# Optimization experiments

Hardware: AMD Instinct MI355X
Metric: run time of the kernel (lower is better)

The kernel has to match this reference:

```python
import jax, jax.numpy as jnp
import numpy as np

MIN_CURV = 1e-06
MIN_NORM = 1e-15

def _norm(x):
    return jnp.clip(jnp.linalg.norm(x, axis=-1, keepdims=True), MIN_NORM, None)

def lorentz_expmap0(v, c):
    sqrt_c = jnp.sqrt(c)
    vn = _norm(v)
    x0 = jnp.cosh(sqrt_c * vn) / sqrt_c
    xs = jnp.sinh(sqrt_c * vn) * v / (sqrt_c * vn)
    return jnp.concatenate([x0, xs], axis=-1)

def lorentz_logmap0(x, c):
    sqrt_c = jnp.sqrt(c)
    x0 = x[..., 0:1]
    xs = x[..., 1:]
    xs_norm = _norm(xs)
    theta = jnp.arccosh(jnp.clip(sqrt_c * x0, 1.0 + 1e-07, None))
    return theta / (sqrt_c * xs_norm) * xs

def lorentz_project(x, c):
    spatial = x[..., 1:]
    sq = jnp.sum(spatial * spatial, axis=-1, keepdims=True)
    x0 = jnp.clip(jnp.sqrt(sq + 1.0 / c), MIN_NORM, None)
    return jnp.concatenate([x0, spatial], axis=-1)

def givens_rotation(x, angles):
    x0 = x[..., 0:1]
    xs = x[..., 1:]
    cos_a = jnp.cos(angles)
    sin_a = jnp.sin(angles)
    xe = xs[..., 0::2]
    xo = xs[..., 1::2]
    ne = cos_a * xe - sin_a * xo
    no = sin_a * xe + cos_a * xo
    xr = jnp.stack([ne, no], axis=-1).reshape(xs.shape)
    return jnp.concatenate([x0, xr], axis=-1)

def setup_inputs() -> dict:
    key = jax.random.key(0)
    ks = jax.random.split(key, 16)
    N_NODE, E, B = 50000, 500000, 64
    IN_DIM, OUT_DIM, ATTN_DIM, N_REL = 128, 128, 128, 200
    N_EMB = 2 * N_REL + 1  # 401
    hidden = jax.random.normal(ks[0], (N_NODE, IN_DIM), dtype=jnp.float32)
    q_sub = jax.random.randint(ks[1], (B,), 0, N_NODE)
    q_rel = jax.random.randint(ks[2], (B,), 0, N_EMB)
    r_idx = jax.random.randint(ks[3], (E,), 0, B)
    rel = jax.random.randint(ks[4], (E,), 0, N_EMB)
    sub = jax.random.randint(ks[5], (E,), 0, N_NODE)
    obj = jax.random.randint(ks[6], (E,), 0, N_NODE)
    zeros = jnp.zeros((E,), dtype=jnp.int32)
    edges = jnp.stack([r_idx, zeros, rel, zeros, sub, obj], axis=1)
    rela_embed = jax.random.normal(ks[7], (N_EMB, IN_DIM), dtype=jnp.float32)
    rel_angles = jax.random.uniform(ks[8], (N_EMB, IN_DIM // 2), minval=-0.1, maxval=0.1, dtype=jnp.float32)
    curvature = jnp.array(1.0, dtype=jnp.float32)
    Ws_w = jax.random.normal(ks[9], (ATTN_DIM, IN_DIM), dtype=jnp.float32) * 0.05
    Wr_w = jax.random.normal(ks[10], (ATTN_DIM, IN_DIM), dtype=jnp.float32) * 0.05
    Wqr_w = jax.random.normal(ks[11], (ATTN_DIM, IN_DIM), dtype=jnp.float32) * 0.05
    Wqr_b = jax.random.normal(ks[12], (ATTN_DIM,), dtype=jnp.float32) * 0.05
    Wattn_w = jax.random.normal(ks[13], (1, ATTN_DIM), dtype=jnp.float32) * 0.05
    Wh_w = jax.random.normal(ks[14], (OUT_DIM, IN_DIM), dtype=jnp.float32) * 0.05
    return {"hidden": hidden, "rela_embed": rela_embed, "rel_angles": rel_angles,
            "curvature": curvature, "Ws_w": Ws_w, "Wr_w": Wr_w, "Wqr_w": Wqr_w,
            "Wqr_b": Wqr_b, "Wattn_w": Wattn_w, "Wh_w": Wh_w,
            "q_sub": q_sub, "q_rel": q_rel, "edges": edges,
            "n_node": N_NODE, "old_nodes_new_idx": jnp.arange(N_NODE)}

def reference(hidden, rela_embed, rel_angles, curvature, Ws_w, Wr_w, Wqr_w, Wqr_b,
              Wattn_w, Wh_w, q_sub, q_rel, edges, n_node, old_nodes_new_idx):
    sub = edges[:, 4]
    rel = edges[:, 2]
    obj = edges[:, 5]
    r_idx = edges[:, 0]
    hs = hidden[sub]                      # [E, in_dim]
    hr = rela_embed[rel]                  # [E, in_dim]
    h_qr = rela_embed[q_rel][r_idx]       # [E, in_dim]
    pre = jax.nn.relu(hs @ Ws_w.T + hr @ Wr_w.T + h_qr @ Wqr_w.T + Wqr_b)
    alpha = jax.nn.sigmoid(pre @ Wattn_w.T)  # [E, 1]
    c = jnp.clip(curvature, MIN_CURV, None)
    mess_tangent = hs + hr
    mess_L = lorentz_expmap0(mess_tangent, c)          # [E, in_dim+1]
    mess_L = givens_rotation(mess_L, rel_angles[rel])
    mess2 = lorentz_logmap0(mess_L, c)                 # [E, in_dim]
    message = mess2 * alpha
    message_agg = jax.ops.segment_sum(message, obj, num_segments=n_node)
    a = message_agg @ Wh_w.T                           # [n_node, out_dim]
    a_L = lorentz_expmap0(a, c)
    # act is identity; project back to hyperboloid and log-map
    a_L = lorentz_project(jnp.concatenate([a_L[..., 0:1], a_L[..., 1:]], axis=-1), c)
    hidden_new = lorentz_logmap0(a_L, c)
    return hidden_new
```

## Files before the change

### kernel.cpp

```cpp
#include <hip/hip_runtime.h>
#include <math.h>

#define D 128
#define CAP 36
#define NQ 64

typedef _Float16 f16x8 __attribute__((ext_vector_type(8)));
typedef _Float16 f16x4 __attribute__((ext_vector_type(4)));
typedef _Float16 f16x2 __attribute__((ext_vector_type(2)));
typedef float    f32x4 __attribute__((ext_vector_type(4)));

union H8 { f16x8 v; f16x4 q[2]; f16x2 p[4]; _Float16 f[8]; };
union H4 { f16x4 v; f16x2 p[2]; _Float16 f[4]; };
union U2 { f16x2 v; unsigned u; };

__device__ __forceinline__ float fdot2f(f16x2 a, f16x2 b, float c){
  return __builtin_amdgcn_fdot2(a, b, c, false);
}
__device__ __forceinline__ f16x2 relu2(f16x2 x){
  f16x2 r;
  r[0] = x[0] > (_Float16)0 ? x[0] : (_Float16)0;
  r[1] = x[1] > (_Float16)0 ? x[1] : (_Float16)0;
  return r;
}
__device__ __forceinline__ f16x2 negHi(f16x2 x){
  U2 u; u.v = x; u.u ^= 0x80000000u; return u.v;
}
__device__ __forceinline__ f16x2 swapH(f16x2 x){
  U2 u; u.v = x; u.u = (u.u >> 16) | (u.u << 16); return u.v;
}


__device__ __forceinline__ void hgemm_core16(const _Float16* __restrict__ A,
                                             const _Float16* __restrict__ W,
                                             int arow, f32x4 acc[8], int quad, int lo){
  #pragma unroll
  for (int kt=0;kt<4;kt++){
    f16x8 a = *(const f16x8*)(A + (size_t)arow*D + kt*32 + quad*8);
    #pragma unroll
    for (int nt=0;nt<8;nt++){
      f16x8 b = *(const f16x8*)(W + (size_t)(nt*16 + lo)*D + kt*32 + quad*8);
      acc[nt] = __builtin_amdgcn_mfma_f32_16x16x32_f16(a, b, acc[nt], 0, 0, 0);
    }
  }
}

__device__ __forceinline__ void store_wpart(_Float16* __restrict__ O, f32x4 acc[8],
                                            int m0, int quad, int lo, int M){
  int r0 = m0 + quad*4;
  #pragma unroll
  for (int i=0;i<4;i++){
    int r = r0 + i;
    if (r < M){
      H4 s1, s2;
      #pragma unroll
      for (int nt=0;nt<4;nt++){
        s1.f[nt] = (_Float16)acc[nt][i];
        s2.f[nt] = (_Float16)acc[nt+4][i];
      }
      *(f16x4*)(O + (size_t)r*256 + lo*16 + 4)  = s1.v;
      *(f16x4*)(O + (size_t)r*256 + lo*16 + 12) = s2.v;
    }
  }
}

__global__ __launch_bounds__(256) void k_prep(
    const float* __restrict__ rela, const float* __restrict__ rel_angles,
    const float* __restrict__ Ws, const float* __restrict__ Wr,
    const float* __restrict__ Wh, const float* __restrict__ Wqr,
    _Float16* __restrict__ rela16, _Float16* __restrict__ relhq,
    _Float16* __restrict__ relcs, _Float16* __restrict__ Ws16,
    _Float16* __restrict__ Wr16, _Float16* __restrict__ Wh16,
    _Float16* __restrict__ Wqr16, int* __restrict__ cnt,
    int NEMB, int NN){
  int idx = blockIdx.x*256 + threadIdx.x;
  int T1 = NEMB*32;
  if (idx < T1){
    int r = idx >> 5, l = idx & 31;
    float4 hv = *(const float4*)(rela + (size_t)r*D + l*4);
    f16x4 h = { (_Float16)hv.x, (_Float16)hv.y, (_Float16)hv.z, (_Float16)hv.w };
    *(f16x4*)(rela16 + (size_t)r*D + l*4) = h;
    *(f16x4*)(relhq  + (size_t)r*256 + l*8) = h;
    float2 an = *(const float2*)(rel_angles + (size_t)r*(D/2) + l*2);
    float c0 = cosf(an.x), s0 = sinf(an.x);
    float c1 = cosf(an.y), s1 = sinf(an.y);
    H4 cs;
    cs.f[0]=(_Float16)c0; cs.f[1]=(_Float16)s0;
    cs.f[2]=(_Float16)c1; cs.f[3]=(_Float16)s1;
    *(f16x4*)(relcs + (size_t)r*128 + l*4) = cs.v;
    return;
  }
  int j = idx - T1;
  if (j < 4*D*D/4){
    const float* src = (j < 4096) ? Ws : (j < 8192) ? Wr : (j < 12288) ? Wh : Wqr;
    _Float16*    dst = (j < 4096) ? Ws16 : (j < 8192) ? Wr16 : (j < 12288) ? Wh16 : Wqr16;
    int o = (j & 4095)*4;
    float4 v = *(const float4*)(src + o);
    f16x4 h = { (_Float16)v.x, (_Float16)v.y, (_Float16)v.z, (_Float16)v.w };
    *(f16x4*)(dst + o) = h;
    return;
  }
  j -= 4*D*D/4;
  if (j < NN + NQ*64) cnt[j] = 0;
}

__global__ __launch_bounds__(256) void k_mega(
    const int* __restrict__ edges, int* __restrict__ cnt, int* __restrict__ bucket,
    int E, const float* __restrict__ hidden, const _Float16* __restrict__ Ws16,
    _Float16* __restrict__ hw16, int NN,
    const _Float16* __restrict__ rela16, const _Float16* __restrict__ Wr16,
    _Float16* __restrict__ relhq, int NEMB, int SB, int GH, int G1,
    const _Float16* __restrict__ Wqr16, const float* __restrict__ Wqr_b,
    const int* __restrict__ q_rel, _Float16* __restrict__ hqw16){
  int b = blockIdx.x;
  if (b < SB){
    int e0 = (b*256 + threadIdx.x)*4;
    if (e0 >= E) return;
    if (e0 + 3 < E){
      const int4* q = (const int4*)(edges + (size_t)e0*6);
      int4 q0=q[0], q1=q[1], q2=q[2], q3=q[3], q4=q[4], q5=q[5];
      int key0 = q1.x | (q0.z << 17) | (q0.x << 26);
      int key1 = q2.z | (q2.x << 17) | (q1.z << 26);
      int key2 = q4.x | (q3.z << 17) | (q3.x << 26);
      int key3 = q5.z | (q5.x << 17) | (q4.z << 26);
      int p0 = atomicAdd(cnt + q1.y, 1);
      int p1 = atomicAdd(cnt + q2.w, 1);
      int p2 = atomicAdd(cnt + q4.y, 1);
      int p3 = atomicAdd(cnt + q5.w, 1);
      if (p0 < CAP) bucket[q1.y*CAP + p0] = key0;
      if (p1 < CAP) bucket[q2.w*CAP + p1] = key1;
      if (p2 < CAP) bucket[q4.y*CAP + p2] = key2;
      if (p3 < CAP) bucket[q5.w*CAP + p3] = key3;
    } else {
      for (int u=0; u<4; u++){
        int e = e0 + u;
        if (e < E){
          const int* er = edges + (size_t)e*6;
          int key = er[4] | (er[2] << 17) | (er[0] << 26);
          int pos = atomicAdd(cnt + er[5], 1);
          if (pos < CAP) bucket[er[5]*CAP + pos] = key;
        }
      }
    }
  } else if (b < SB + GH){
    int bb = b - SB;
    int wave = threadIdx.x >> 6;
    int lane = threadIdx.x & 63;
    int quad = lane >> 4, lo = lane & 15;
    int m0 = bb*64 + wave*16;
    int arow = min(m0 + lo, NN-1);
    f32x4 acc[8];
    #pragma unroll
    for (int nt=0;nt<8;nt++) acc[nt] = (f32x4){0.f,0.f,0.f,0.f};
    H8 hpack[4];
    #pragma unroll
    for (int kt=0;kt<4;kt++){
      float4 a0 = *(const float4*)(hidden + (size_t)arow*D + kt*32 + quad*8);
      float4 a1 = *(const float4*)(hidden + (size_t)arow*D + kt*32 + quad*8 + 4);
      H8 a;
      a.f[0]=(_Float16)a0.x; a.f[1]=(_Float16)a0.y; a.f[2]=(_Float16)a0.z; a.f[3]=(_Float16)a0.w;
      a.f[4]=(_Float16)a1.x; a.f[5]=(_Float16)a1.y; a.f[6]=(_Float16)a1.z; a.f[7]=(_Float16)a1.w;
      hpack[kt] = a;
      #pragma unroll
      for (int nt=0;nt<8;nt++){
        f16x8 bb2 = *(const f16x8*)(Ws16 + (size_t)(nt*16 + lo)*D + kt*32 + quad*8);
        acc[nt] = __builtin_amdgcn_mfma_f32_16x16x32_f16(a.v, bb2, acc[nt], 0, 0, 0);
      }
    }
    if (m0 + lo < NN){
      #pragma unroll
      for (int kt=0;kt<4;kt++){
        int g = kt*8 + quad*2;
        *(f16x4*)(hw16 + (size_t)arow*256 + g*8)     = hpack[kt].q[0];
        *(f16x4*)(hw16 + (size_t)arow*256 + (g+1)*8) = hpack[kt].q[1];
      }
    }
    store_wpart(hw16, acc, m0, quad, lo, NN);
  } else if (b < SB + GH + G1){
    int bb = b - SB - GH;
    int wave = threadIdx.x >> 6;
    int lane = threadIdx.x & 63;
    int quad = lane >> 4, lo = lane & 15;
    int m0 = bb*64 + wave*16;
    int arow = min(m0 + lo, NEMB-1);
    f32x4 acc[8];
    #pragma unroll
    for (int nt=0;nt<8;nt++) acc[nt] = (f32x4){0.f,0.f,0.f,0.f};
    hgemm_core16(rela16, Wr16, arow, acc, quad, lo);
    store_wpart(relhq, acc, m0, quad, lo, NEMB);
  } else {
    int wave = threadIdx.x >> 6;
    int lane = threadIdx.x & 63;
    int quad = lane >> 4, lo = lane & 15;
    int m0 = wave*16;
    int arow = q_rel[m0 + lo];
    f32x4 acc[8];
    #pragma unroll
    for (int nt=0;nt<8;nt++) acc[nt] = (f32x4){0.f,0.f,0.f,0.f};
    hgemm_core16(rela16, Wqr16, arow, acc, quad, lo);
    int r0 = m0 + quad*4;
    #pragma unroll
    for (int nt=0;nt<8;nt++){
      int c = nt*16 + lo;
      float bia = Wqr_b[c];
      int p = ((c & 15) << 3) + (c >> 4);
      #pragma unroll
      for (int i=0;i<4;i++){
        int r = r0 + i;
        hqw16[r*128 + p] = (_Float16)(acc[nt][i] + bia);
      }
    }
  }
}

struct P {
  H8 h0,h1,h2,h3;
  int4 q;
  float m1,m2,m3;
};

__device__ __forceinline__ void pload(const int* __restrict__ bk, int g, int deg,
    const _Float16* __restrict__ hw16, unsigned lh8, P& o){
  int4 q = *(const int4*)(bk + (g << 2));
  int base = g << 2;
  bool v1 = base + 1 < deg, v2 = base + 2 < deg, v3 = base + 3 < deg;
  if (!v1) q.y = 0;
  if (!v2) q.z = 0;
  if (!v3) q.w = 0;
  o.q = q;
  o.m1 = v1 ? 1.f : 0.f;
  o.m2 = v2 ? 1.f : 0.f;
  o.m3 = v3 ? 1.f : 0.f;
  o.h0.v = *(const f16x8*)(hw16 + ((((unsigned)q.x) & 0x1FFFF) << 8) + lh8);
  o.h1.v = *(const f16x8*)(hw16 + ((((unsigned)q.y) & 0x1FFFF) << 8) + lh8);
  o.h2.v = *(const f16x8*)(hw16 + ((((unsigned)q.z) & 0x1FFFF) << 8) + lh8);
  o.h3.v = *(const f16x8*)(hw16 + ((((unsigned)q.w) & 0x1FFFF) << 8) + lh8);
}

__device__ __forceinline__ void gcompute(const P& A,
    const _Float16* __restrict__ relcs, const _Float16* __restrict__ relhq,
    const _Float16* shq,
    unsigned lh8, unsigned lh4, int l, f16x2 wa01, f16x2 wa23,
    float& ax, float& ay, float& az, float& aw){
  unsigned r0 = ((unsigned)A.q.x >> 17) & 0x1FF, i0 = (unsigned)A.q.x >> 26;
  unsigned r1 = ((unsigned)A.q.y >> 17) & 0x1FF, i1 = (unsigned)A.q.y >> 26;
  unsigned r2 = ((unsigned)A.q.z >> 17) & 0x1FF, i2 = (unsigned)A.q.z >> 26;
  unsigned r3 = ((unsigned)A.q.w >> 17) & 0x1FF, i3 = (unsigned)A.q.w >> 26;
  H4 c0,c1,c2,c3; H8 e0,e1,e2,e3; H4 w0,w1,w2,w3;
  c0.v = *(const f16x4*)(relcs + (r0 << 7) + lh4);
  c1.v = *(const f16x4*)(relcs + (r1 << 7) + lh4);
  c2.v = *(const f16x4*)(relcs + (r2 << 7) + lh4);
  c3.v = *(const f16x4*)(relcs + (r3 << 7) + lh4);
  e0.v = *(const f16x8*)(relhq + (r0 << 8) + lh8);
  e1.v = *(const f16x8*)(relhq + (r1 << 8) + lh8);
  e2.v = *(const f16x8*)(relhq + (r2 << 8) + lh8);
  e3.v = *(const f16x8*)(relhq + (r3 << 8) + lh8);
  w0.v = *(const f16x4*)(shq + (i0 << 7) + lh4);
  w1.v = *(const f16x4*)(shq + (i1 << 7) + lh4);
  w2.v = *(const f16x4*)(shq + (i2 << 7) + lh4);
  w3.v = *(const f16x4*)(shq + (i3 << 7) + lh4);
  f16x2 ta, tb;
  ta = relu2(A.h0.p[2] + e0.p[2] + w0.p[0]); tb = relu2(A.h0.p[3] + e0.p[3] + w0.p[1]);
  float s0 = fdot2f(ta, wa01, fdot2f(tb, wa23, 0.f));
  ta = relu2(A.h1.p[2] + e1.p[2] + w1.p[0]); tb = relu2(A.h1.p[3] + e1.p[3] + w1.p[1]);
  float s1 = fdot2f(ta, wa01, fdot2f(tb, wa23, 0.f));
  ta = relu2(A.h2.p[2] + e2.p[2] + w2.p[0]); tb = relu2(A.h2.p[3] + e2.p[3] + w2.p[1]);
  float s2 = fdot2f(ta, wa01, fdot2f(tb, wa23, 0.f));
  ta = relu2(A.h3.p[2] + e3.p[2] + w3.p[0]); tb = relu2(A.h3.p[3] + e3.p[3] + w3.p[1]);
  float s3 = fdot2f(ta, wa01, fdot2f(tb, wa23, 0.f));
  bool b0 = (l & 1) != 0, b1 = (l & 2) != 0;
  float x01 = b0 ? s1 : s0, y01 = b0 ? s0 : s1;
  float r01 = x01 + __shfl_xor(y01, 1);
  float x23 = b0 ? s3 : s2, y23 = b0 ? s2 : s3;
  float r23 = x23 + __shfl_xor(y23, 1);
  float xa = b1 ? r23 : r01, ya = b1 ? r01 : r23;
  float rr = xa + __shfl_xor(ya, 2);
  rr += __shfl_xor(rr, 4);
  rr += __shfl_xor(rr, 8);
  rr += __shfl_xor(rr, 16);
  float av = __builtin_amdgcn_rcpf(1.f + __expf(-rr));
  float aB = __shfl_xor(av, 1);
  float aC = __shfl_xor(av, 2);
  float aD = __shfl_xor(aB, 2);
  float g0 = b0 ? aB : av, g1 = b0 ? av : aB, g2 = b0 ? aD : aC, g3 = b0 ? aC : aD;
  float al0 = b1 ? g2 : g0, al1 = b1 ? g3 : g1, al2 = b1 ? g0 : g2, al3 = b1 ? g1 : g3;
  al1 *= A.m1; al2 *= A.m2; al3 *= A.m3;
  f16x2 v01, v23;
  v01 = A.h0.p[0] + e0.p[0]; v23 = A.h0.p[1] + e0.p[1];
  float dx0 = fdot2f(negHi(c0.p[0]), v01, 0.f), dy0 = fdot2f(swapH(c0.p[0]), v01, 0.f);
  float dz0 = fdot2f(negHi(c0.p[1]), v23, 0.f), dw0 = fdot2f(swapH(c0.p[1]), v23, 0.f);
  v01 = A.h1.p[0] + e1.p[0]; v23 = A.h1.p[1] + e1.p[1];
  float dx1 = fdot2f(negHi(c1.p[0]), v01, 0.f), dy1 = fdot2f(swapH(c1.p[0]), v01, 0.f);
  float dz1 = fdot2f(negHi(c1.p[1]), v23, 0.f), dw1 = fdot2f(swapH(c1.p[1]), v23, 0.f);
  v01 = A.h2.p[0] + e2.p[0]; v23 = A.h2.p[1] + e2.p[1];
  float dx2 = fdot2f(negHi(c2.p[0]), v01, 0.f), dy2 = fdot2f(swapH(c2.p[0]), v01, 0.f);
  float dz2 = fdot2f(negHi(c2.p[1]), v23, 0.f), dw2 = fdot2f(swapH(c2.p[1]), v23, 0.f);
  v01 = A.h3.p[0] + e3.p[0]; v23 = A.h3.p[1] + e3.p[1];
  float dx3 = fdot2f(negHi(c3.p[0]), v01, 0.f), dy3 = fdot2f(swapH(c3.p[0]), v01, 0.f);
  float dz3 = fdot2f(negHi(c3.p[1]), v23, 0.f), dw3 = fdot2f(swapH(c3.p[1]), v23, 0.f);
  ax += al0*dx0 + al1*dx1 + al2*dx2 + al3*dx3;
  ay += al0*dy0 + al1*dy1 + al2*dy2 + al3*dy3;
  az += al0*dz0 + al1*dz1 + al2*dz2 + al3*dz3;
  aw += al0*dw0 + al1*dw1 + al2*dw2 + al3*dw3;
}

__global__ __launch_bounds__(256, 4) void k_aggregate(
    const _Float16* __restrict__ hw16, const _Float16* __restrict__ relcs,
    const _Float16* __restrict__ relhq, const _Float16* __restrict__ hqw16,
    const float* __restrict__ Wattn, const int* __restrict__ cnt,
    const int* __restrict__ bucket, _Float16* __restrict__ agg16, int NN,
    int* __restrict__ wq, int B){
  __shared__ _Float16 shq[64*128];
  int t = threadIdx.x;
  int nb = min(B, 64) * 128;
  for (int i = t*8; i < nb; i += 256*8)
    *(f16x8*)(shq + i) = *(const f16x8*)(hqw16 + i);
  __syncthreads();

  int l = t & 31;
  unsigned lh8 = (unsigned)l*8, lh4 = (unsigned)l*4;
  unsigned p0 = (unsigned)l*4;
  float w0 = Wattn[(((p0+0)&7)<<4) + ((p0+0)>>3)];
  float w1 = Wattn[(((p0+1)&7)<<4) + ((p0+1)>>3)];
  float w2 = Wattn[(((p0+2)&7)<<4) + ((p0+2)>>3)];
  float w3 = Wattn[(((p0+3)&7)<<4) + ((p0+3)>>3)];
  f16x2 wa01 = { (_Float16)w0, (_Float16)w1 };
  f16x2 wa23 = { (_Float16)w2, (_Float16)w3 };

  int cid  = blockIdx.x & (NQ-1);
  int qpc  = NN / NQ, rem = NN % NQ;
  int base = cid * qpc + min(cid, rem);
  int len  = qpc + (cid < rem ? 1 : 0);
  int* myq = wq + cid * 64;

  for (;;){
    int i;
    if (l == 0) i = atomicAdd(myq, 1);
    i = __shfl(i, 0, 32);
    if (i >= len) break;
    int n = base + i;

    int deg = min(cnt[n], CAP);
    const int* bk = bucket + n*CAP;
    float ax=0.f, ay=0.f, az=0.f, aw=0.f;

    int ng = (deg + 3) >> 2;
    if (ng){
      P A, Bf;
      pload(bk, 0, deg, hw16, lh8, A);
      int g = 0;
      for (;;){
        if (g + 1 < ng) pload(bk, g+1, deg, hw16, lh8, Bf);
        gcompute(A, relcs, relhq, shq, lh8, lh4, l, wa01, wa23, ax, ay, az, aw);
        if (++g >= ng) break;
        if (g + 1 < ng) pload(bk, g+1, deg, hw16, lh8, A);
        gcompute(Bf, relcs, relhq, shq, lh8, lh4, l, wa01, wa23, ax, ay, az, aw);
        if (++g >= ng) break;
      }
    }

    f16x4 o = { (_Float16)ax, (_Float16)ay, (_Float16)az, (_Float16)aw };
    *(f16x4*)(agg16 + ((size_t)n << 7) + lh4) = o;
  }
}

__global__ __launch_bounds__(256) void k_hgemm0(const _Float16* __restrict__ A,
                                                const _Float16* __restrict__ W,
                                                float* __restrict__ O, int M){
  int wave = threadIdx.x >> 6;
  int lane = threadIdx.x & 63;
  int quad = lane >> 4, lo = lane & 15;
  int m0 = blockIdx.x*64 + wave*16;
  int arow = min(m0 + lo, M-1);
  f32x4 acc[8];
  #pragma unroll
  for (int nt=0;nt<8;nt++) acc[nt] = (f32x4){0.f,0.f,0.f,0.f};
  hgemm_core16(A, W, arow, acc, quad, lo);
  int r0 = m0 + quad*4;
  #pragma unroll
  for (int nt=0;nt<8;nt++){
    int c = nt*16 + lo;
    #pragma unroll
    for (int i=0;i<4;i++){
      int r = r0 + i;
      if (r < M) O[(size_t)r*D + c] = acc[nt][i];
    }
  }
}

extern "C" void kernel_launch(void* const* d_in, const int* in_sizes, int n_in,
                              void* d_out, int out_size, void* d_ws, size_t ws_size,
                              hipStream_t stream){
  const float* hidden     = (const float*)d_in[0];
  const float* rela       = (const float*)d_in[1];
  const float* rel_angles = (const float*)d_in[2];
  const float* Ws         = (const float*)d_in[4];
  const float* Wr         = (const float*)d_in[5];
  const float* Wqr        = (const float*)d_in[6];
  const float* Wqr_b      = (const float*)d_in[7];
  const float* Wattn      = (const float*)d_in[8];
  const float* Wh         = (const float*)d_in[9];
  const int*   q_rel      = (const int*)d_in[11];
  const int*   edges      = (const int*)d_in[12];

  int NN   = in_sizes[0] / D;
  int NEMB = in_sizes[1] / D;
  int B    = in_sizes[11];
  int E    = in_sizes[12] / 6;

  char* p = (char*)d_ws;
  auto alloc = [&](size_t bytes)->char*{
    char* r = p; p += (bytes + 255) & ~(size_t)255; return r;
  };
  _Float16* hw16   = (_Float16*)alloc((size_t)NN*256*2);
  _Float16* agg16  = (_Float16*)alloc((size_t)NN*D*2);
  _Float16* rela16 = (_Float16*)alloc((size_t)NEMB*D*2);
  _Float16* relhq  = (_Float16*)alloc((size_t)NEMB*256*2);
  _Float16* relcs  = (_Float16*)alloc((size_t)NEMB*128*2);
  _Float16* hqw16  = (_Float16*)alloc((size_t)B*D*2);
  _Float16* Ws16   = (_Float16*)alloc((size_t)D*D*2);
  _Float16* Wr16   = (_Float16*)alloc((size_t)D*D*2);
  _Float16* Wh16   = (_Float16*)alloc((size_t)D*D*2);
  _Float16* Wqr16  = (_Float16*)alloc((size_t)D*D*2);
  int*      cnt    = (int*)alloc((size_t)(NN + NQ*64)*4);
  int*      bucket = (int*)alloc((size_t)NN*CAP*4);

  int smallN = NEMB*32 + 4*D*D/4 + NN + NQ*64;
  int PA = (smallN + 255)/256;
  k_prep<<<PA, 256, 0, stream>>>(rela, rel_angles, Ws, Wr, Wh, Wqr,
                                 rela16, relhq, relcs, Ws16, Wr16, Wh16,
                                 Wqr16, cnt, NEMB, NN);

  int SB = (E + 1023)/1024;
  int GH = (NN + 63)/64;
  int G1 = (NEMB + 63)/64;
  k_mega<<<SB + GH + G1 + 1, 256, 0, stream>>>(edges, cnt, bucket, E, hidden,
                                               Ws16, hw16, NN, rela16, Wr16,
                                               relhq, NEMB, SB, GH, G1,
                                               Wqr16, Wqr_b, q_rel, hqw16);

  k_aggregate<<<2048, 256, 0, stream>>>(hw16, relcs, relhq, hqw16,
                                        Wattn, cnt, bucket, agg16, NN,
                                        cnt + NN, B);
  k_hgemm0<<<(NN+63)/64, 256, 0, stream>>>(agg16, Wh16, (float*)d_out, NN);
}
```

Baseline: 225.3 us.

## Split edge scatter out of merged GEMM kernel into separate launch

Moves the edge bucketing scatter out of the combined mega kernel into its own kernel, launched just before a kernel that holds only the three GEMM branches. The scatter now handles one edge per thread with scalar loads, where it used to handle four edges per thread with int4 vector loads. This separates the atomic-heavy scatter from the MFMA GEMM blocks, possibly to avoid interference or register-pressure coupling between them. In exchange it adds a kernel launch and serializes work that used to run concurrently in one grid.

```diff
diff --git a/kernel.cpp b/kernel.cpp
--- a/kernel.cpp
+++ b/kernel.cpp
@@ -104,50 +104,31 @@
   if (j < NN + NQ*64) cnt[j] = 0;
 }
 
-__global__ __launch_bounds__(256) void k_mega(
-    const int* __restrict__ edges, int* __restrict__ cnt, int* __restrict__ bucket,
-    int E, const float* __restrict__ hidden, const _Float16* __restrict__ Ws16,
+__global__ __launch_bounds__(256) void k_scatter(
+    const int* __restrict__ edges, int* __restrict__ cnt,
+    int* __restrict__ bucket, int E){
+  int e = blockIdx.x*256 + threadIdx.x;
+  if (e >= E) return;
+  const int* er = edges + (size_t)e*6;
+  int key = er[4] | (er[2] << 17) | (er[0] << 26);
+  int obj = er[5];
+  int pos = atomicAdd(cnt + obj, 1);
+  if (pos < CAP) bucket[obj*CAP + pos] = key;
+}
+
+__global__ __launch_bounds__(256) void k_gemms(
+    const float* __restrict__ hidden, const _Float16* __restrict__ Ws16,
     _Float16* __restrict__ hw16, int NN,
     const _Float16* __restrict__ rela16, const _Float16* __restrict__ Wr16,
-    _Float16* __restrict__ relhq, int NEMB, int SB, int GH, int G1,
+    _Float16* __restrict__ relhq, int NEMB, int GH, int G1,
     const _Float16* __restrict__ Wqr16, const float* __restrict__ Wqr_b,
     const int* __restrict__ q_rel, _Float16* __restrict__ hqw16){
   int b = blockIdx.x;
-  if (b < SB){
-    int e0 = (b*256 + threadIdx.x)*4;
-    if (e0 >= E) return;
-    if (e0 + 3 < E){
-      const int4* q = (const int4*)(edges + (size_t)e0*6);
-      int4 q0=q[0], q1=q[1], q2=q[2], q3=q[3], q4=q[4], q5=q[5];
-      int key0 = q1.x | (q0.z << 17) | (q0.x << 26);
-      int key1 = q2.z | (q2.x << 17) | (q1.z << 26);
-      int key2 = q4.x | (q3.z << 17) | (q3.x << 26);
-      int key3 = q5.z | (q5.x << 17) | (q4.z << 26);
-      int p0 = atomicAdd(cnt + q1.y, 1);
-      int p1 = atomicAdd(cnt + q2.w, 1);
-      int p2 = atomicAdd(cnt + q4.y, 1);
-      int p3 = atomicAdd(cnt + q5.w, 1);
-      if (p0 < CAP) bucket[q1.y*CAP + p0] = key0;
-      if (p1 < CAP) bucket[q2.w*CAP + p1] = key1;
-      if (p2 < CAP) bucket[q4.y*CAP + p2] = key2;
-      if (p3 < CAP) bucket[q5.w*CAP + p3] = key3;
-    } else {
-      for (int u=0; u<4; u++){
-        int e = e0 + u;
-        if (e < E){
-          const int* er = edges + (size_t)e*6;
-          int key = er[4] | (er[2] << 17) | (er[0] << 26);
-          int pos = atomicAdd(cnt + er[5], 1);
-          if (pos < CAP) bucket[er[5]*CAP + pos] = key;
-        }
-      }
-    }
-  } else if (b < SB + GH){
-    int bb = b - SB;
+  if (b < GH){
     int wave = threadIdx.x >> 6;
     int lane = threadIdx.x & 63;
     int quad = lane >> 4, lo = lane & 15;
-    int m0 = bb*64 + wave*16;
+    int m0 = b*64 + wave*16;
     int arow = min(m0 + lo, NN-1);
     f32x4 acc[8];
     #pragma unroll
@@ -176,8 +157,8 @@
       }
     }
     store_wpart(hw16, acc, m0, quad, lo, NN);
-  } else if (b < SB + GH + G1){
-    int bb = b - SB - GH;
+  } else if (b < GH + G1){
+    int bb = b - GH;
     int wave = threadIdx.x >> 6;
     int lane = threadIdx.x & 63;
     int quad = lane >> 4, lo = lane & 15;
@@ -431,13 +412,12 @@
                                  rela16, relhq, relcs, Ws16, Wr16, Wh16,
                                  Wqr16, cnt, NEMB, NN);
 
-  int SB = (E + 1023)/1024;
   int GH = (NN + 63)/64;
   int G1 = (NEMB + 63)/64;
-  k_mega<<<SB + GH + G1 + 1, 256, 0, stream>>>(edges, cnt, bucket, E, hidden,
-                                               Ws16, hw16, NN, rela16, Wr16,
-                                               relhq, NEMB, SB, GH, G1,
-                                               Wqr16, Wqr_b, q_rel, hqw16);
+  k_scatter<<<(E + 255)/256, 256, 0, stream>>>(edges, cnt, bucket, E);
+  k_gemms<<<GH + G1 + 1, 256, 0, stream>>>(hidden, Ws16, hw16, NN, rela16,
+                                           Wr16, relhq, NEMB, GH, G1,
+                                           Wqr16, Wqr_b, q_rel, hqw16);
 
   k_aggregate<<<2048, 256, 0, stream>>>(hw16, relcs, relhq, hqw16,
                                         Wattn, cnt, bucket, agg16, NN,
```

Result: no change. 227.9 us (+1.2%).
